# Kernel tuning notes

Measured on AMD Instinct MI355X. Metric: run time of the kernel, lower is better.

The kernel has to match this reference:

```python
import jax, jax.numpy as jnp
import numpy as np

B, N, D, D_MODEL = 4, 2048, 512, 512


def setup_inputs() -> dict:
    key = jax.random.key(0)
    kx, kq, kk, kv, ks = jax.random.split(key, 5)
    scale = 1.0 / np.sqrt(D)
    x = jax.random.normal(kx, (B, N, D), dtype=jnp.float32)
    Wq = (jax.random.normal(kq, (D, D_MODEL), dtype=jnp.float32) * scale)
    Wk = (jax.random.normal(kk, (D, D_MODEL), dtype=jnp.float32) * scale)
    Wv = (jax.random.normal(kv, (D, D_MODEL), dtype=jnp.float32) * scale)
    Ws = (jax.random.normal(ks, (D, 1), dtype=jnp.float32) * scale)
    return {"x": x, "Wq": Wq, "Wk": Wk, "Wv": Wv, "Ws": Ws}


def reference(x, Wq, Wk, Wv, Ws):
    # Projections (Linear, no bias)
    Q = x @ Wq                      # (B, N, d_model)
    K = x @ Wk                      # (B, N, d_model)
    V = x @ Wv                      # (B, N, d_model)
    sigma = x @ Ws                  # (B, N, 1)

    n = x.shape[1]
    dm = Wq.shape[1]

    # Prior association: Gaussian kernel over |i-j| distance, row-normalized
    idx = jnp.arange(n)
    dist = jnp.abs(idx[:, None] - idx[None, :]).astype(x.dtype)      # (N, N)
    inv_norm = 1.0 / (jnp.sqrt(2.0 * jnp.pi).astype(x.dtype) * jnp.abs(sigma))
    gaussian = inv_norm * jnp.exp(-0.5 * jnp.square(dist[None] / sigma))  # (B,N,N)
    P = gaussian / jnp.sum(gaussian, axis=-1, keepdims=True)

    # Series association: scaled dot-product softmax attention
    scores = jnp.einsum('bnd,bmd->bnm', Q, K) / jnp.sqrt(jnp.asarray(dm, x.dtype))
    S = jax.nn.softmax(scores, axis=-1)                               # (B,N,N)

    # Reconstruction
    Z = S @ V                                                          # (B,N,d_model)
    return (Z, P)
```

## Files before the change

### kernel.cpp

```cpp
#include <hip/hip_runtime.h>

typedef float f32x4 __attribute__((ext_vector_type(4)));
typedef short s16x8 __attribute__((ext_vector_type(8)));
typedef unsigned short us4 __attribute__((ext_vector_type(4)));

#define MFMA16(a, b, c) __builtin_amdgcn_mfma_f32_16x16x32_bf16(a, b, c, 0, 0, 0)

#define GLOAD_LDS16(gp, lp) __builtin_amdgcn_global_load_lds( \
    (__attribute__((address_space(1))) void*)(gp),            \
    (__attribute__((address_space(3))) void*)(lp), 16, 0, 0)

__device__ __forceinline__ unsigned short f2bf(float f) {
    union { float f; unsigned u; } v; v.f = f;
    unsigned r = v.u + 0x7fffu + ((v.u >> 16) & 1u);
    return (unsigned short)(r >> 16);
}

__device__ __forceinline__ void gemm_core128(
    const unsigned short* __restrict__ Ab, size_t Astride,
    const unsigned short* __restrict__ Bb, size_t Bstride,
    int K, unsigned short* As, unsigned short* Bs,
    int t, f32x4 acc[4][4])
{
    const int wave = t >> 6, lane = t & 63;
    const int c = lane & 15, quad = lane >> 4;
    const int wm = (wave >> 1) * 64, wn = (wave & 1) * 64;
    const int srow = t >> 2;
    const int scol = (t & 3) * 8;

    for (int k0 = 0; k0 < K; k0 += 32) {
        __syncthreads();
        const unsigned short* ga = Ab + (size_t)srow * Astride + k0 + scol;
        const unsigned short* gb = Bb + (size_t)srow * Bstride + k0 + scol;
        GLOAD_LDS16(ga,                 As + t * 8);
        GLOAD_LDS16(ga + 64 * Astride,  As + 2048 + t * 8);
        GLOAD_LDS16(gb,                 Bs + t * 8);
        GLOAD_LDS16(gb + 64 * Bstride,  Bs + 2048 + t * 8);
        __syncthreads();

        s16x8 af[4], bfr[4];
        #pragma unroll
        for (int i = 0; i < 4; i++)
            af[i] = *(const s16x8*)(As + (wm + i * 16 + c) * 32 + quad * 8);
        #pragma unroll
        for (int i = 0; i < 4; i++)
            bfr[i] = *(const s16x8*)(Bs + (wn + i * 16 + c) * 32 + quad * 8);
        #pragma unroll
        for (int mt = 0; mt < 4; mt++)
            #pragma unroll
            for (int nt = 0; nt < 4; nt++)
                acc[mt][nt] = MFMA16(af[mt], bfr[nt], acc[mt][nt]);
    }
}

__global__ __launch_bounds__(256) void k_convert(
    const float* __restrict__ x, const float* __restrict__ wq,
    const float* __restrict__ wk, const float* __restrict__ wv,
    unsigned short* __restrict__ xbf, unsigned short* __restrict__ wt,
    float* __restrict__ lg)
{
    int bid = blockIdx.x, t = threadIdx.x;
    if (bid < 4096) {
        int gid = bid * 256 + t;
        float4 v = ((const float4*)x)[gid];
        us4 o = { f2bf(v.x), f2bf(v.y), f2bf(v.z), f2bf(v.w) };
        ((us4*)xbf)[gid] = o;
    } else if (bid < 7168) {
        int idx = (bid - 4096) * 256 + t;
        int w = idx >> 18;
        int r = idx & 262143;
        int k = r >> 9, n = r & 511;
        const float* src = (w == 0) ? wq : (w == 1) ? wk : wv;
        wt[((size_t)(w * 512 + n) << 9) + k] = f2bf(src[r]);
    } else {
        lg[(bid - 7168) * 256 + t] = 0.f;
    }
}

__global__ __launch_bounds__(256) void k_proj(
    const unsigned short* __restrict__ xbf, const unsigned short* __restrict__ wt,
    unsigned short* __restrict__ qbf, unsigned short* __restrict__ kbf,
    unsigned short* __restrict__ vtbf)
{
    __shared__ __align__(16) unsigned short As[128 * 32];
    __shared__ __align__(16) unsigned short Bs[128 * 32];

    int t = threadIdx.x;
    int wave = t >> 6, lane = t & 63, c = lane & 15, quad = lane >> 4;
    int wm = (wave >> 1) * 64, wn = (wave & 1) * 64;
    f32x4 acc[4][4] = {};

    if (blockIdx.y < 8) {
        int m0 = blockIdx.y * 128;
        int tok0 = blockIdx.x * 128;
        gemm_core128(wt + (size_t)m0 * 512, 512, xbf + (size_t)tok0 * 512, 512,
                     512, As, Bs, t, acc);

        unsigned short* dst = (m0 < 512) ? qbf : kbf;
        int mbase = m0 & 511;
        #pragma unroll
        for (int mt = 0; mt < 4; mt++) {
            int dim0 = mbase + wm + mt * 16 + quad * 4;
            #pragma unroll
            for (int nt = 0; nt < 4; nt++) {
                int token = tok0 + wn + nt * 16 + c;
                us4 pk = { f2bf(acc[mt][nt][0]), f2bf(acc[mt][nt][1]),
                           f2bf(acc[mt][nt][2]), f2bf(acc[mt][nt][3]) };
                *(us4*)(dst + (size_t)token * 512 + dim0) = pk;
            }
        }
    } else {
        int m0 = blockIdx.x * 128;
        int n0 = 1024 + (blockIdx.y - 8) * 128;
        gemm_core128(xbf + (size_t)m0 * 512, 512, wt + (size_t)n0 * 512, 512,
                     512, As, Bs, t, acc);

        #pragma unroll
        for (int mt = 0; mt < 4; mt++) {
            int rw0 = m0 + wm + mt * 16 + quad * 4;
            int bb = rw0 >> 11, nn = rw0 & 2047;
            #pragma unroll
            for (int nt = 0; nt < 4; nt++) {
                int d = (n0 - 1024) + wn + nt * 16 + c;
                us4 pk = { f2bf(acc[mt][nt][0]), f2bf(acc[mt][nt][1]),
                           f2bf(acc[mt][nt][2]), f2bf(acc[mt][nt][3]) };
                *(us4*)(vtbf + ((size_t)(bb * 512 + d)) * 2048 + nn) = pk;
            }
        }
    }
}

__device__ __forceinline__ void score_body(
    const unsigned short* __restrict__ qbf, const unsigned short* __restrict__ kbf,
    unsigned short* __restrict__ pbf, float* __restrict__ lg,
    int b, int kt0, int q0, int t, unsigned short* As, unsigned short* Bs)
{
    f32x4 acc[4][4] = {};
    gemm_core128(kbf + (size_t)(b * 2048 + kt0) * 512, 512,
                 qbf + (size_t)(b * 2048 + q0) * 512, 512,
                 512, As, Bs, t, acc);

    int wave = t >> 6, lane = t & 63, c = lane & 15, quad = lane >> 4;
    int wm = (wave >> 1) * 64, wn = (wave & 1) * 64;
    const float scale = 0.044194173824159216f;

    #pragma unroll
    for (int nt = 0; nt < 4; nt++) {
        int q = q0 + wn + nt * 16 + c;
        float rs = 0.f;
        unsigned short* pr = pbf + (size_t)(b * 2048 + q) * 2048 + kt0 + wm + quad * 4;
        #pragma unroll
        for (int mt = 0; mt < 4; mt++) {
            us4 pk;
            #pragma unroll
            for (int r = 0; r < 4; r++) {
                float p = __expf(acc[mt][nt][r] * scale);
                rs += p;
                pk[r] = f2bf(p);
            }
            *(us4*)(pr + mt * 16) = pk;
        }
        rs += __shfl_xor(rs, 16);
        rs += __shfl_xor(rs, 32);
        if (quad == 0) atomicAdd(&lg[b * 2048 + q], rs);
    }
}

__device__ __forceinline__ void prior_body(
    const float* __restrict__ x, const float* __restrict__ wsv,
    float* __restrict__ pout, int blk, int t, float* red, float* red2)
{
    int i = blk & 2047;
    const float* xr = x + (size_t)blk * 512;

    float part = xr[t] * wsv[t] + xr[t + 256] * wsv[t + 256];
    #pragma unroll
    for (int o = 32; o; o >>= 1) part += __shfl_xor(part, o, 64);
    if ((t & 63) == 0) red[t >> 6] = part;
    __syncthreads();
    float sigma = red[0] + red[1] + red[2] + red[3];

    float inv2 = 0.5f / (sigma * sigma);
    float g[8];
    float sum = 0.f;
    int j0 = t * 8;
    #pragma unroll
    for (int u = 0; u < 8; u++) {
        int j = j0 + u;
        float d = (float)(j - i);
        g[u] = (j == i) ? 1.0f : __expf(-(d * d) * inv2);
        sum += g[u];
    }
    #pragma unroll
    for (int o = 32; o; o >>= 1) sum += __shfl_xor(sum, o, 64);
    if ((t & 63) == 0) red2[t >> 6] = sum;
    __syncthreads();
    float inv = 1.0f / (red2[0] + red2[1] + red2[2] + red2[3]);

    float* pr = pout + (size_t)blk * 2048 + j0;
    float4 o0 = { g[0] * inv, g[1] * inv, g[2] * inv, g[3] * inv };
    float4 o1 = { g[4] * inv, g[5] * inv, g[6] * inv, g[7] * inv };
    ((float4*)pr)[0] = o0;
    ((float4*)pr)[1] = o1;
}

__global__ __launch_bounds__(256) void k_score_prior(
    const unsigned short* __restrict__ qbf, const unsigned short* __restrict__ kbf,
    unsigned short* __restrict__ pbf, float* __restrict__ lg,
    const float* __restrict__ x, const float* __restrict__ wsv,
    float* __restrict__ pout)
{
    __shared__ __align__(16) unsigned short As[128 * 32];
    __shared__ __align__(16) unsigned short Bs[128 * 32];
    __shared__ float red[4];
    __shared__ float red2[4];

    int bid = blockIdx.x, t = threadIdx.x;
    if (bid < 1024) {
        int b = bid >> 8, r = bid & 255;
        score_body(qbf, kbf, pbf, lg, b, (r & 15) * 128, (r >> 4) * 128, t, As, Bs);
    } else {
        prior_body(x, wsv, pout, bid - 1024, t, red, red2);
    }
}

__global__ __launch_bounds__(256) void k_score(
    const unsigned short* __restrict__ qbf, const unsigned short* __restrict__ kbf,
    unsigned short* __restrict__ pbf, float* __restrict__ lg)
{
    __shared__ __align__(16) unsigned short As[128 * 32];
    __shared__ __align__(16) unsigned short Bs[128 * 32];
    score_body(qbf, kbf, pbf, lg, blockIdx.z,
               blockIdx.x * 128, blockIdx.y * 128, threadIdx.x, As, Bs);
}

__global__ __launch_bounds__(256) void k_out(
    const unsigned short* __restrict__ pbf, const unsigned short* __restrict__ vtbf,
    const float* __restrict__ lg, float* __restrict__ zout)
{
    __shared__ __align__(16) unsigned short As[64 * 32];
    __shared__ __align__(16) unsigned short Bs[128 * 32];
    __shared__ float invl[128];

    int t = threadIdx.x;
    int b = blockIdx.z;
    int d0 = blockIdx.x * 64, q0 = blockIdx.y * 128;

    if (t < 128) invl[t] = 1.0f / lg[b * 2048 + q0 + t];

    const unsigned short* Ab = vtbf + (size_t)(b * 512 + d0) * 2048;
    const unsigned short* Bb = pbf + (size_t)(b * 2048 + q0) * 2048;

    const int wave = t >> 6, lane = t & 63;
    const int c = lane & 15, quad = lane >> 4;
    const int wm = (wave >> 1) * 32, wn = (wave & 1) * 64;
    const int srow = t >> 2;
    const int scol = (t & 3) * 8;

    f32x4 acc[2][4] = {};

    for (int k0 = 0; k0 < 2048; k0 += 32) {
        __syncthreads();
        GLOAD_LDS16(Ab + (size_t)srow * 2048 + k0 + scol, As + t * 8);
        const unsigned short* gb = Bb + (size_t)srow * 2048 + k0 + scol;
        GLOAD_LDS16(gb,             Bs + t * 8);
        GLOAD_LDS16(gb + 64 * 2048, Bs + 2048 + t * 8);
        __syncthreads();

        s16x8 af[2], bfr[4];
        #pragma unroll
        for (int i = 0; i < 2; i++)
            af[i] = *(const s16x8*)(As + (wm + i * 16 + c) * 32 + quad * 8);
        #pragma unroll
        for (int i = 0; i < 4; i++)
            bfr[i] = *(const s16x8*)(Bs + (wn + i * 16 + c) * 32 + quad * 8);
        #pragma unroll
        for (int mt = 0; mt < 2; mt++)
            #pragma unroll
            for (int nt = 0; nt < 4; nt++)
                acc[mt][nt] = MFMA16(af[mt], bfr[nt], acc[mt][nt]);
    }

    #pragma unroll
    for (int mt = 0; mt < 2; mt++) {
        int dd = wm + mt * 16 + quad * 4;
        #pragma unroll
        for (int nt = 0; nt < 4; nt++) {
            int qi = wn + nt * 16 + c;
            float il = invl[qi];
            float4 o = { acc[mt][nt][0] * il, acc[mt][nt][1] * il,
                         acc[mt][nt][2] * il, acc[mt][nt][3] * il };
            *(float4*)(zout + (size_t)(b * 2048 + q0 + qi) * 512 + d0 + dd) = o;
        }
    }
}

__global__ __launch_bounds__(256) void k_prior(
    const float* __restrict__ x, const float* __restrict__ wsv,
    float* __restrict__ pout)
{
    __shared__ float red[4];
    __shared__ float red2[4];
    prior_body(x, wsv, pout, blockIdx.x, threadIdx.x, red, red2);
}

extern "C" void kernel_launch(void* const* d_in, const int* in_sizes, int n_in,
                              void* d_out, int out_size, void* d_ws, size_t ws_size,
                              hipStream_t stream)
{
    const float* x  = (const float*)d_in[0];
    const float* wq = (const float*)d_in[1];
    const float* wk = (const float*)d_in[2];
    const float* wv = (const float*)d_in[3];
    const float* ws = (const float*)d_in[4];

    float* zout = (float*)d_out;
    float* pout = zout + (size_t)4 * 2048 * 512;

    const size_t need = ((size_t)4194304 + 786432 + 3 * 4194304 + 16777216) * 2
                        + 8192 * 4;

    if (ws_size >= need) {
        unsigned short* base = (unsigned short*)d_ws;
        unsigned short* xbf  = base;
        unsigned short* wt   = xbf  + (size_t)4194304;
        unsigned short* qbf  = wt   + (size_t)786432;
        unsigned short* kbf  = qbf  + (size_t)4194304;
        unsigned short* vtbf = kbf  + (size_t)4194304;
        unsigned short* pbf  = vtbf + (size_t)4194304;
        float*          lg   = (float*)(pbf + (size_t)16777216);

        k_convert<<<dim3(7200), dim3(256), 0, stream>>>(x, wq, wk, wv, xbf, wt, lg);
        k_proj       <<<dim3(64, 12),   dim3(256), 0, stream>>>(xbf, wt, qbf, kbf, vtbf);
        k_score_prior<<<dim3(9216),     dim3(256), 0, stream>>>(qbf, kbf, pbf, lg, x, ws, pout);
        k_out        <<<dim3(8, 16, 4), dim3(256), 0, stream>>>(pbf, vtbf, lg, zout);
    } else {
        unsigned short* base = (unsigned short*)pout;
        unsigned short* pbf  = base;
        unsigned short* qbf  = base + (size_t)16777216;
        unsigned short* kbf  = qbf  + (size_t)4194304;
        unsigned short* vtbf = kbf  + (size_t)4194304;
        float*          lg   = (float*)(vtbf + (size_t)4194304);
        unsigned short* xbf  = base;
        unsigned short* wt   = base + (size_t)4194304;

        k_convert<<<dim3(7200), dim3(256), 0, stream>>>(x, wq, wk, wv, xbf, wt, lg);
        k_proj  <<<dim3(64, 12),    dim3(256), 0, stream>>>(xbf, wt, qbf, kbf, vtbf);
        k_score <<<dim3(16, 16, 4), dim3(256), 0, stream>>>(qbf, kbf, pbf, lg);
        k_out   <<<dim3(8, 16, 4),  dim3(256), 0, stream>>>(pbf, vtbf, lg, zout);
        k_prior <<<dim3(8192),      dim3(256), 0, stream>>>(x, ws, pout);
    }
}
```

Before: 215.1 us.

## Use BK=64 swizzled LDS tiles and fuse prior into projection kernel

```diff
diff --git a/kernel.cpp b/kernel.cpp
--- a/kernel.cpp
+++ b/kernel.cpp
@@ -16,7 +16,7 @@
     return (unsigned short)(r >> 16);
 }
 
-__device__ __forceinline__ void gemm_core128(
+__device__ __forceinline__ void gemm_core128_bk64(
     const unsigned short* __restrict__ Ab, size_t Astride,
     const unsigned short* __restrict__ Bb, size_t Bstride,
     int K, unsigned short* As, unsigned short* Bs,
@@ -25,31 +25,38 @@
     const int wave = t >> 6, lane = t & 63;
     const int c = lane & 15, quad = lane >> 4;
     const int wm = (wave >> 1) * 64, wn = (wave & 1) * 64;
-    const int srow = t >> 2;
-    const int scol = (t & 3) * 8;
-
-    for (int k0 = 0; k0 < K; k0 += 32) {
+
+    for (int k0 = 0; k0 < K; k0 += 64) {
         __syncthreads();
-        const unsigned short* ga = Ab + (size_t)srow * Astride + k0 + scol;
-        const unsigned short* gb = Bb + (size_t)srow * Bstride + k0 + scol;
-        GLOAD_LDS16(ga,                 As + t * 8);
-        GLOAD_LDS16(ga + 64 * Astride,  As + 2048 + t * 8);
-        GLOAD_LDS16(gb,                 Bs + t * 8);
-        GLOAD_LDS16(gb + 64 * Bstride,  Bs + 2048 + t * 8);
+        #pragma unroll
+        for (int i = 0; i < 4; i++) {
+            int idx = i * 256 + t;
+            int row = idx >> 3;
+            int sch = (idx & 7) ^ (row & 7);
+            GLOAD_LDS16(Ab + (size_t)row * Astride + k0 + sch * 8, As + idx * 8);
+            GLOAD_LDS16(Bb + (size_t)row * Bstride + k0 + sch * 8, Bs + idx * 8);
+        }
         __syncthreads();
 
-        s16x8 af[4], bfr[4];
-        #pragma unroll
-        for (int i = 0; i < 4; i++)
-            af[i] = *(const s16x8*)(As + (wm + i * 16 + c) * 32 + quad * 8);
-        #pragma unroll
-        for (int i = 0; i < 4; i++)
-            bfr[i] = *(const s16x8*)(Bs + (wn + i * 16 + c) * 32 + quad * 8);
-        #pragma unroll
-        for (int mt = 0; mt < 4; mt++)
-            #pragma unroll
-            for (int nt = 0; nt < 4; nt++)
-                acc[mt][nt] = MFMA16(af[mt], bfr[nt], acc[mt][nt]);
+        #pragma unroll
+        for (int s = 0; s < 2; s++) {
+            s16x8 af[4], bfr[4];
+            #pragma unroll
+            for (int i = 0; i < 4; i++) {
+                int r = wm + i * 16 + c;
+                af[i] = *(const s16x8*)(As + r * 64 + (((s << 2) | quad) ^ (r & 7)) * 8);
+            }
+            #pragma unroll
+            for (int i = 0; i < 4; i++) {
+                int r = wn + i * 16 + c;
+                bfr[i] = *(const s16x8*)(Bs + r * 64 + (((s << 2) | quad) ^ (r & 7)) * 8);
+            }
+            #pragma unroll
+            for (int mt = 0; mt < 4; mt++)
+                #pragma unroll
+                for (int nt = 0; nt < 4; nt++)
+                    acc[mt][nt] = MFMA16(af[mt], bfr[nt], acc[mt][nt]);
+        }
     }
 }
 
@@ -77,24 +84,72 @@
     }
 }
 
+__device__ __forceinline__ void prior_body(
+    const float* __restrict__ x, const float* __restrict__ wsv,
+    float* __restrict__ pout, int blk, int t, float* red, float* red2)
+{
+    int i = blk & 2047;
+    const float* xr = x + (size_t)blk * 512;
+
+    float part = xr[t] * wsv[t] + xr[t + 256] * wsv[t + 256];
+    #pragma unroll
+    for (int o = 32; o; o >>= 1) part += __shfl_xor(part, o, 64);
+    if ((t & 63) == 0) red[t >> 6] = part;
+    __syncthreads();
+    float sigma = red[0] + red[1] + red[2] + red[3];
+
+    float inv2 = 0.5f / (sigma * sigma);
+    float g[8];
+    float sum = 0.f;
+    int j0 = t * 8;
+    #pragma unroll
+    for (int u = 0; u < 8; u++) {
+        int j = j0 + u;
+        float d = (float)(j - i);
+        g[u] = (j == i) ? 1.0f : __expf(-(d * d) * inv2);
+        sum += g[u];
+    }
+    #pragma unroll
+    for (int o = 32; o; o >>= 1) sum += __shfl_xor(sum, o, 64);
+    if ((t & 63) == 0) red2[t >> 6] = sum;
+    __syncthreads();
+    float inv = 1.0f / (red2[0] + red2[1] + red2[2] + red2[3]);
+
+    float* pr = pout + (size_t)blk * 2048 + j0;
+    float4 o0 = { g[0] * inv, g[1] * inv, g[2] * inv, g[3] * inv };
+    float4 o1 = { g[4] * inv, g[5] * inv, g[6] * inv, g[7] * inv };
+    ((float4*)pr)[0] = o0;
+    ((float4*)pr)[1] = o1;
+}
+
 __global__ __launch_bounds__(256) void k_proj(
     const unsigned short* __restrict__ xbf, const unsigned short* __restrict__ wt,
     unsigned short* __restrict__ qbf, unsigned short* __restrict__ kbf,
-    unsigned short* __restrict__ vtbf)
-{
-    __shared__ __align__(16) unsigned short As[128 * 32];
-    __shared__ __align__(16) unsigned short Bs[128 * 32];
-
-    int t = threadIdx.x;
+    unsigned short* __restrict__ vtbf,
+    const float* __restrict__ x, const float* __restrict__ wsv,
+    float* __restrict__ pout)
+{
+    __shared__ __align__(16) unsigned short As[128 * 64];
+    __shared__ __align__(16) unsigned short Bs[128 * 64];
+    __shared__ float red[4];
+    __shared__ float red2[4];
+
+    int bid = blockIdx.x, t = threadIdx.x;
+    if (bid >= 768) {
+        prior_body(x, wsv, pout, bid - 768, t, red, red2);
+        return;
+    }
+
+    int bx = bid & 63, by = bid >> 6;
     int wave = t >> 6, lane = t & 63, c = lane & 15, quad = lane >> 4;
     int wm = (wave >> 1) * 64, wn = (wave & 1) * 64;
     f32x4 acc[4][4] = {};
 
-    if (blockIdx.y < 8) {
-        int m0 = blockIdx.y * 128;
-        int tok0 = blockIdx.x * 128;
-        gemm_core128(wt + (size_t)m0 * 512, 512, xbf + (size_t)tok0 * 512, 512,
-                     512, As, Bs, t, acc);
+    if (by < 8) {
+        int m0 = by * 128;
+        int tok0 = bx * 128;
+        gemm_core128_bk64(wt + (size_t)m0 * 512, 512, xbf + (size_t)tok0 * 512, 512,
+                          512, As, Bs, t, acc);
 
         unsigned short* dst = (m0 < 512) ? qbf : kbf;
         int mbase = m0 & 511;
@@ -110,10 +165,10 @@
             }
         }
     } else {
-        int m0 = blockIdx.x * 128;
-        int n0 = 1024 + (blockIdx.y - 8) * 128;
-        gemm_core128(xbf + (size_t)m0 * 512, 512, wt + (size_t)n0 * 512, 512,
-                     512, As, Bs, t, acc);
+        int m0 = bx * 128;
+        int n0 = 1024 + (by - 8) * 128;
+        gemm_core128_bk64(xbf + (size_t)m0 * 512, 512, wt + (size_t)n0 * 512, 512,
+                          512, As, Bs, t, acc);
 
         #pragma unroll
         for (int mt = 0; mt < 4; mt++) {
@@ -130,15 +185,21 @@
     }
 }
 
-__device__ __forceinline__ void score_body(
+__global__ __launch_bounds__(256) void k_score(
     const unsigned short* __restrict__ qbf, const unsigned short* __restrict__ kbf,
-    unsigned short* __restrict__ pbf, float* __restrict__ lg,
-    int b, int kt0, int q0, int t, unsigned short* As, unsigned short* Bs)
-{
+    unsigned short* __restrict__ pbf, float* __restrict__ lg)
+{
+    __shared__ __align__(16) unsigned short As[128 * 64];
+    __shared__ __align__(16) unsigned short Bs[128 * 64];
+
+    int t = threadIdx.x;
+    int b = blockIdx.z;
+    int kt0 = blockIdx.x * 128, q0 = blockIdx.y * 128;
+
     f32x4 acc[4][4] = {};
-    gemm_core128(kbf + (size_t)(b * 2048 + kt0) * 512, 512,
-                 qbf + (size_t)(b * 2048 + q0) * 512, 512,
-                 512, As, Bs, t, acc);
+    gemm_core128_bk64(kbf + (size_t)(b * 2048 + kt0) * 512, 512,
+                      qbf + (size_t)(b * 2048 + q0) * 512, 512,
+                      512, As, Bs, t, acc);
 
     int wave = t >> 6, lane = t & 63, c = lane & 15, quad = lane >> 4;
     int wm = (wave >> 1) * 64, wn = (wave & 1) * 64;
@@ -166,80 +227,12 @@
     }
 }
 
-__device__ __forceinline__ void prior_body(
-    const float* __restrict__ x, const float* __restrict__ wsv,
-    float* __restrict__ pout, int blk, int t, float* red, float* red2)
-{
-    int i = blk & 2047;
-    const float* xr = x + (size_t)blk * 512;
-
-    float part = xr[t] * wsv[t] + xr[t + 256] * wsv[t + 256];
-    #pragma unroll
-    for (int o = 32; o; o >>= 1) part += __shfl_xor(part, o, 64);
-    if ((t & 63) == 0) red[t >> 6] = part;
-    __syncthreads();
-    float sigma = red[0] + red[1] + red[2] + red[3];
-
-    float inv2 = 0.5f / (sigma * sigma);
-    float g[8];
-    float sum = 0.f;
-    int j0 = t * 8;
-    #pragma unroll
-    for (int u = 0; u < 8; u++) {
-        int j = j0 + u;
-        float d = (float)(j - i);
-        g[u] = (j == i) ? 1.0f : __expf(-(d * d) * inv2);
-        sum += g[u];
-    }
-    #pragma unroll
-    for (int o = 32; o; o >>= 1) sum += __shfl_xor(sum, o, 64);
-    if ((t & 63) == 0) red2[t >> 6] = sum;
-    __syncthreads();
-    float inv = 1.0f / (red2[0] + red2[1] + red2[2] + red2[3]);
-
-    float* pr = pout + (size_t)blk * 2048 + j0;
-    float4 o0 = { g[0] * inv, g[1] * inv, g[2] * inv, g[3] * inv };
-    float4 o1 = { g[4] * inv, g[5] * inv, g[6] * inv, g[7] * inv };
-    ((float4*)pr)[0] = o0;
-    ((float4*)pr)[1] = o1;
-}
-
-__global__ __launch_bounds__(256) void k_score_prior(
-    const unsigned short* __restrict__ qbf, const unsigned short* __restrict__ kbf,
-    unsigned short* __restrict__ pbf, float* __restrict__ lg,
-    const float* __restrict__ x, const float* __restrict__ wsv,
-    float* __restrict__ pout)
-{
-    __shared__ __align__(16) unsigned short As[128 * 32];
-    __shared__ __align__(16) unsigned short Bs[128 * 32];
-    __shared__ float red[4];
-    __shared__ float red2[4];
-
-    int bid = blockIdx.x, t = threadIdx.x;
-    if (bid < 1024) {
-        int b = bid >> 8, r = bid & 255;
-        score_body(qbf, kbf, pbf, lg, b, (r & 15) * 128, (r >> 4) * 128, t, As, Bs);
-    } else {
-        prior_body(x, wsv, pout, bid - 1024, t, red, red2);
-    }
-}
-
-__global__ __launch_bounds__(256) void k_score(
-    const unsigned short* __restrict__ qbf, const unsigned short* __restrict__ kbf,
-    unsigned short* __restrict__ pbf, float* __restrict__ lg)
-{
-    __shared__ __align__(16) unsigned short As[128 * 32];
-    __shared__ __align__(16) unsigned short Bs[128 * 32];
-    score_body(qbf, kbf, pbf, lg, blockIdx.z,
-               blockIdx.x * 128, blockIdx.y * 128, threadIdx.x, As, Bs);
-}
-
 __global__ __launch_bounds__(256) void k_out(
     const unsigned short* __restrict__ pbf, const unsigned short* __restrict__ vtbf,
     const float* __restrict__ lg, float* __restrict__ zout)
 {
-    __shared__ __align__(16) unsigned short As[64 * 32];
-    __shared__ __align__(16) unsigned short Bs[128 * 32];
+    __shared__ __align__(16) unsigned short As[64 * 64];
+    __shared__ __align__(16) unsigned short Bs[128 * 64];
     __shared__ float invl[128];
 
     int t = threadIdx.x;
@@ -254,31 +247,46 @@
     const int wave = t >> 6, lane = t & 63;
     const int c = lane & 15, quad = lane >> 4;
     const int wm = (wave >> 1) * 32, wn = (wave & 1) * 64;
-    const int srow = t >> 2;
-    const int scol = (t & 3) * 8;
 
     f32x4 acc[2][4] = {};
 
-    for (int k0 = 0; k0 < 2048; k0 += 32) {
+    for (int k0 = 0; k0 < 2048; k0 += 64) {
         __syncthreads();
-        GLOAD_LDS16(Ab + (size_t)srow * 2048 + k0 + scol, As + t * 8);
-        const unsigned short* gb = Bb + (size_t)srow * 2048 + k0 + scol;
-        GLOAD_LDS16(gb,             Bs + t * 8);
-        GLOAD_LDS16(gb + 64 * 2048, Bs + 2048 + t * 8);
+        #pragma unroll
+        for (int i = 0; i < 2; i++) {
+            int idx = i * 256 + t;
+            int row = idx >> 3;
+            int sch = (idx & 7) ^ (row & 7);
+            GLOAD_LDS16(Ab + (size_t)row * 2048 + k0 + sch * 8, As + idx * 8);
+        }
+        #pragma unroll
+        for (int i = 0; i < 4; i++) {
+            int idx = i * 256 + t;
+            int row = idx >> 3;
+            int sch = (idx & 7) ^ (row & 7);
+            GLOAD_LDS16(Bb + (size_t)row * 2048 + k0 + sch * 8, Bs + idx * 8);
+        }
         __syncthreads();
 
-        s16x8 af[2], bfr[4];
-        #pragma unroll
-        for (int i = 0; i < 2; i++)
-            af[i] = *(const s16x8*)(As + (wm + i * 16 + c) * 32 + quad * 8);
-        #pragma unroll
-        for (int i = 0; i < 4; i++)
-            bfr[i] = *(const s16x8*)(Bs + (wn + i * 16 + c) * 32 + quad * 8);
-        #pragma unroll
-        for (int mt = 0; mt < 2; mt++)
-            #pragma unroll
-            for (int nt = 0; nt < 4; nt++)
-                acc[mt][nt] = MFMA16(af[mt], bfr[nt], acc[mt][nt]);
+        #pragma unroll
+        for (int s = 0; s < 2; s++) {
+            s16x8 af[2], bfr[4];
+            #pragma unroll
+            for (int i = 0; i < 2; i++) {
+                int r = wm + i * 16 + c;
+                af[i] = *(const s16x8*)(As + r * 64 + (((s << 2) | quad) ^ (r & 7)) * 8);
+            }
+            #pragma unroll
+            for (int i = 0; i < 4; i++) {
+                int r = wn + i * 16 + c;
+                bfr[i] = *(const s16x8*)(Bs + r * 64 + (((s << 2) | quad) ^ (r & 7)) * 8);
+            }
+            #pragma unroll
+            for (int mt = 0; mt < 2; mt++)
+                #pragma unroll
+                for (int nt = 0; nt < 4; nt++)
+                    acc[mt][nt] = MFMA16(af[mt], bfr[nt], acc[mt][nt]);
+        }
     }
 
     #pragma unroll
@@ -331,9 +339,10 @@
         float*          lg   = (float*)(pbf + (size_t)16777216);
 
         k_convert<<<dim3(7200), dim3(256), 0, stream>>>(x, wq, wk, wv, xbf, wt, lg);
-        k_proj       <<<dim3(64, 12),   dim3(256), 0, stream>>>(xbf, wt, qbf, kbf, vtbf);
-        k_score_prior<<<dim3(9216),     dim3(256), 0, stream>>>(qbf, kbf, pbf, lg, x, ws, pout);
-        k_out        <<<dim3(8, 16, 4), dim3(256), 0, stream>>>(pbf, vtbf, lg, zout);
+        k_proj <<<dim3(768 + 8192), dim3(256), 0, stream>>>(xbf, wt, qbf, kbf, vtbf,
+                                                            x, ws, pout);
+        k_score<<<dim3(16, 16, 4),  dim3(256), 0, stream>>>(qbf, kbf, pbf, lg);
+        k_out  <<<dim3(8, 16, 4),   dim3(256), 0, stream>>>(pbf, vtbf, lg, zout);
     } else {
         unsigned short* base = (unsigned short*)pout;
         unsigned short* pbf  = base;
@@ -345,9 +354,10 @@
         unsigned short* wt   = base + (size_t)4194304;
 
         k_convert<<<dim3(7200), dim3(256), 0, stream>>>(x, wq, wk, wv, xbf, wt, lg);
-        k_proj  <<<dim3(64, 12),    dim3(256), 0, stream>>>(xbf, wt, qbf, kbf, vtbf);
-        k_score <<<dim3(16, 16, 4), dim3(256), 0, stream>>>(qbf, kbf, pbf, lg);
-        k_out   <<<dim3(8, 16, 4),  dim3(256), 0, stream>>>(pbf, vtbf, lg, zout);
-        k_prior <<<dim3(8192),      dim3(256), 0, stream>>>(x, ws, pout);
-    }
-}
+        k_proj <<<dim3(768),       dim3(256), 0, stream>>>(xbf, wt, qbf, kbf, vtbf,
+                                                           x, ws, pout);
+        k_score<<<dim3(16, 16, 4), dim3(256), 0, stream>>>(qbf, kbf, pbf, lg);
+        k_out  <<<dim3(8, 16, 4),  dim3(256), 0, stream>>>(pbf, vtbf, lg, zout);
+        k_prior<<<dim3(8192),      dim3(256), 0, stream>>>(x, ws, pout);
+    }
+}
```

Measured after the change: 216.3 us. Within noise of the previous version (+0.6%).
